# Kernel tuning notes

Measured on AMD Instinct MI355X. Metric: run time of the kernel, lower is better.

## Reference

```python
import jax, jax.numpy as jnp
import numpy as np

B, L, DIM = 8, 512, 8          # batch, seq len, raw channels (value dim D = 2*DIM = 16)
ET, HID, H = 128, 128, 2       # embed_time, hidden_size, num_heads
MAXLEN = 512
NEG = -1e9


def setup_inputs() -> dict:
    key = jax.random.key(0)
    ks = jax.random.split(key, 40)
    def n(i, shape, s=0.05):
        return jax.random.normal(ks[i], shape, jnp.float32) * s
    vals = jax.random.normal(ks[0], (B, L, DIM), jnp.float32)
    msk = (jax.random.uniform(ks[1], (B, L, DIM)) > 0.2).astype(jnp.float32)
    x = jnp.concatenate([vals, msk], -1)                      # (B, L, 2*DIM)
    time_steps = jax.random.uniform(ks[2], (B, L), jnp.float32)
    return {
        'x': x, 'time_steps': time_steps,
        # learned time embedding: Linear(1, ET-1) periodic + Linear(1,1)
        'w_per': n(3, (1, ET - 1)), 'b_per': n(4, (ET - 1,)),
        'w_lin': n(5, (1, 1)), 'b_lin': n(6, (1,)),
        # MultiTimeAttention projections
        'Wq_t': n(7, (ET, ET)), 'bq_t': n(8, (ET,)),
        'Wk_t': n(9, (ET, ET)), 'bk_t': n(10, (ET,)),
        'Wo_t': n(11, (2 * DIM * H, HID)), 'bo_t': n(12, (HID,)),
        'pos_emb': n(13, (MAXLEN + 1, HID)), 'cls_emb': n(14, (1, HID)),
        # transformer block (BERT-style post-LN encoder layer, d_ff=HID)
        'tWq': n(15, (HID, HID)), 'tbq': n(16, (HID,)),
        'tWk': n(17, (HID, HID)), 'tbk': n(18, (HID,)),
        'tWv': n(19, (HID, HID)), 'tbv': n(20, (HID,)),
        'tWo': n(21, (HID, HID)), 'tbo': n(22, (HID,)),
        'ln1_g': jnp.ones((HID,), jnp.float32), 'ln1_b': jnp.zeros((HID,), jnp.float32),
        'fW1': n(23, (HID, HID)), 'fb1': n(24, (HID,)),
        'fW2': n(25, (HID, HID)), 'fb2': n(26, (HID,)),
        'ln2_g': jnp.ones((HID,), jnp.float32), 'ln2_b': jnp.zeros((HID,), jnp.float32),
        # BertPooler
        'pW': n(27, (HID, HID)), 'pb': n(28, (HID,)),
    }


def _time_emb(tt, w_per, b_per, w_lin, b_lin):
    tt = tt[..., None]                                        # (B, L, 1)
    return jnp.concatenate([tt @ w_lin + b_lin, jnp.sin(tt @ w_per + b_per)], -1)


def _ln(x, g, b, eps=1e-5):
    m = x.mean(-1, keepdims=True)
    v = ((x - m) ** 2).mean(-1, keepdims=True)
    return (x - m) / jnp.sqrt(v + eps) * g + b


def _mta(q_emb, k_emb, value, mask, Wq, bq, Wk, bk, Wo, bo):
    # MultiTimeAttention: scores broadcast to value-channel axis, softmax over keys
    D = value.shape[-1]
    dk = ET // H
    def split(e, W, b):
        p = e @ W + b
        return p.reshape(e.shape[0], -1, H, dk).transpose(0, 2, 1, 3)
    q = split(q_emb, Wq, bq)                                  # (Bq, H, Lq, dk)
    k = split(k_emb, Wk, bk)                                  # (B,  H, Lk, dk)
    scores = jnp.matmul(q, k.swapaxes(-1, -2)) / jnp.sqrt(jnp.float32(dk))  # (B,H,Lq,Lk)
    s5 = jnp.where(mask[:, None, None, :, :] == 0, NEG, scores[..., None])  # (B,H,Lq,Lk,D)
    p = jax.nn.softmax(s5, axis=-2)
    out = jnp.einsum('bhqkd,bkd->bhqd', p, value)             # (B, H, Lq, D)
    Bv = value.shape[0]
    out = out.transpose(0, 2, 1, 3).reshape(Bv, -1, H * D)
    return out @ Wo + bo


def _tblock(x, tWq, tbq, tWk, tbk, tWv, tbv, tWo, tbo, ln1_g, ln1_b,
            fW1, fb1, fW2, fb2, ln2_g, ln2_b):
    Bq, Lq, _ = x.shape
    dk = HID // H
    def heads(W, b):
        return (x @ W + b).reshape(Bq, Lq, H, dk).transpose(0, 2, 1, 3)
    q, k, v = heads(tWq, tbq), heads(tWk, tbk), heads(tWv, tbv)
    a = jax.nn.softmax(jnp.matmul(q, k.swapaxes(-1, -2)) / jnp.sqrt(jnp.float32(dk)), -1)
    o = jnp.matmul(a, v).transpose(0, 2, 1, 3).reshape(Bq, Lq, HID) @ tWo + tbo
    x = _ln(x + o, ln1_g, ln1_b)
    f = jax.nn.relu(x @ fW1 + fb1) @ fW2 + fb2
    return _ln(x + f, ln2_g, ln2_b)


def reference(x, time_steps, w_per, b_per, w_lin, b_lin,
              Wq_t, bq_t, Wk_t, bk_t, Wo_t, bo_t, pos_emb, cls_emb,
              tWq, tbq, tWk, tbk, tWv, tbv, tWo, tbo, ln1_g, ln1_b,
              fW1, fb1, fW2, fb2, ln2_g, ln2_b, pW, pb):
    Bx = x.shape[0]
    mask_half = x[:, :, DIM:]
    mask = jnp.concatenate([mask_half, mask_half], -1)        # (B, L, 2*DIM)
    key_e = _time_emb(time_steps, w_per, b_per, w_lin, b_lin)
    tq_e = _time_emb(time_steps, w_per, b_per, w_lin, b_lin)  # query_time_steps=None -> same
    cls_t = jnp.linspace(0.0, 1.0, 128, dtype=jnp.float32)[None]
    cls_q_e = _time_emb(cls_t, w_per, b_per, w_lin, b_lin)    # (1, 128, ET)
    cls_out = _mta(cls_q_e, key_e, x, mask, Wq_t, bq_t, Wk_t, bk_t, Wo_t, bo_t)
    out = _mta(tq_e, key_e, x, mask, Wq_t, bq_t, Wk_t, bk_t, Wo_t, bo_t)
    tb = (tWq, tbq, tWk, tbk, tWv, tbv, tWo, tbo, ln1_g, ln1_b,
          fW1, fb1, fW2, fb2, ln2_g, ln2_b)
    cls_repr = jnp.broadcast_to(cls_emb[None, :, :], (Bx, 1, HID))
    # encode(cls_out, is_pooling=True), pooling='bert': no pos emb, take token 0
    h = _tblock(jnp.concatenate([cls_repr, cls_out], 1), *tb)
    cls_pooling = jnp.tanh(h[:, 0] @ pW + pb)                 # (B, HID)
    # encode(out, is_pooling=False) [pretrain path]: pos emb + transformer, drop CLS
    h2 = jnp.concatenate([cls_repr, out], 1)                  # (B, L+1, HID)
    h2 = h2 + pos_emb[:h2.shape[1]][None]
    h2 = _tblock(h2, *tb)
    last_hidden_state = h2[:, 1:]                             # (B, L, HID)
    return cls_pooling, last_hidden_state
```

## Files before the change

### kernel.cpp

```cpp
#include <hip/hip_runtime.h>
#include <hip/hip_bf16.h>
#include <math.h>


static constexpr int NM_ = 8 * 513;
static constexpr int NC_ = 8 * 129;
static constexpr int NT_ = NM_ + NC_;

using bf = __hip_bfloat16;
typedef __attribute__((ext_vector_type(8))) short bf16x8;
typedef __attribute__((ext_vector_type(4))) short bf16x4;
typedef __attribute__((ext_vector_type(4))) float floatx4;
typedef __attribute__((ext_vector_type(8))) unsigned short ushortx8;

__device__ __forceinline__ float wave_reduce_sum(float v) {
    #pragma unroll
    for (int off = 32; off >= 1; off >>= 1) v += __shfl_xor(v, off);
    return v;
}
__device__ __forceinline__ float wave_reduce_max(float v) {
    #pragma unroll
    for (int off = 32; off >= 1; off >>= 1) v = fmaxf(v, __shfl_xor(v, off));
    return v;
}
__device__ __forceinline__ float u2f(unsigned short u) {
    return __uint_as_float(((unsigned)u) << 16);
}
__device__ __forceinline__ unsigned short f2u(float f) {
    unsigned u = __float_as_uint(f);
    return (unsigned short)((u + 0x7FFF + ((u >> 16) & 1)) >> 16);
}
__device__ __forceinline__ bf16x8 join8(bf16x4 lo, bf16x4 hi) {
    return __builtin_shufflevector(lo, hi, 0, 1, 2, 3, 4, 5, 6, 7);
}
__device__ __forceinline__ float rdin(const void* p, int i, int flag) {
    return flag ? u2f(((const unsigned short*)p)[i]) : ((const float*)p)[i];
}

struct PrepAll {
    const void* src[32]; int n[32]; int dstoff[32];
    int cstart[32]; int cnum[32];
    int ncv;
    const void* wsrc[8]; unsigned short* wdst[8]; float wscale[8];
    const void* ts; const void* w_per; const void* b_per;
    const void* w_lin; const void* b_lin;
    unsigned short* key_e16;
    unsigned short* btg;
    const void* xsrc;
    const unsigned short* det;
};
__global__ void prep_all_kernel(PrepAll a, float* dst) {
    int flag = (a.det[0] == 0x3F80u) ? 1 : 0;
    int blk = blockIdx.x, tid = threadIdx.x;
    if (blk < a.ncv) {
        int which = -1, bi = 0;
        #pragma unroll
        for (int i = 0; i < 32; ++i)
            if (blk >= a.cstart[i] && blk < a.cstart[i] + a.cnum[i]) { which = i; bi = blk - a.cstart[i]; }
        if (which < 0) return;
        int i = bi * 256 + tid;
        if (i < a.n[which]) dst[a.dstoff[which] + i] = rdin(a.src[which], i, flag);
    } else if (blk < a.ncv + 512) {
        int p = blk - a.ncv;
        int m = p >> 6;
        int idx = (p & 63) * 256 + tid;
        int c = idx >> 9;
        int l = (idx >> 3) & 63;
        int j = idx & 7;
        int k = (c >> 3) * 32 + (l >> 4) * 8 + j;
        int n = (c & 7) * 16 + (l & 15);
        a.wdst[m][idx] = f2u(rdin(a.wsrc[m], k * 128 + n, flag) * a.wscale[m]);
    } else if (blk < a.ncv + 512 + 2112) {
        int p = blk - a.ncv - 512;
        int row = p * 2 + (tid >> 7), j = tid & 127;
        float t = (row < 4096) ? rdin(a.ts, row, flag)
                               : (float)(row - 4096) * (1.0f / 127.0f);
        float v;
        if (j == 0) v = t * rdin(a.w_lin, 0, flag) + rdin(a.b_lin, 0, flag);
        else        v = sinf(t * rdin(a.w_per, j - 1, flag) + rdin(a.b_per, j - 1, flag));
        a.key_e16[row * 128 + j] = f2u(v);
    } else {
        int p = blk - a.ncv - 512 - 2112;
        int e0 = (p * 256 + tid) * 8;
        int b = e0 >> 13;
        int c = (e0 >> 9) & 15;
        int k0 = e0 & 511;
        unsigned short out[8];
        #pragma unroll
        for (int j = 0; j < 8; ++j) {
            int k = k0 + j;
            float m = rdin(a.xsrc, (b * 512 + k) * 16 + 8 + (c & 7), flag);
            float val = (c < 8) ? rdin(a.xsrc, (b * 512 + k) * 16 + c, flag) * m : m;
            out[j] = f2u(val);
        }
        *(ushortx8*)(a.btg + e0) = *(ushortx8*)out;
    }
}

struct GemmM {
    const void* A[3]; const unsigned short* W[3]; const float* bias[3];
    unsigned short* C[3];
    int M[3]; float bscale[3];
};
__global__ void __launch_bounds__(256)
gemm_mfma_kernel(GemmM p) {
    int y = blockIdx.y;
    const unsigned short* Wsw = p.W[y];
    const float* bias = p.bias[y];
    unsigned short* C = p.C[y];
    int M = p.M[y];
    float bscale = p.bscale[y];
    int m0 = blockIdx.x * 16;
    if (m0 >= M) return;
    __shared__ unsigned short As[16][136];
    int tid = threadIdx.x;
    {
        const unsigned short* A = (const unsigned short*)p.A[y];
        int r = tid >> 4, c0 = (tid & 15) * 8;
        ushortx8 v = {0, 0, 0, 0, 0, 0, 0, 0};
        if (m0 + r < M) v = *(const ushortx8*)(A + (size_t)(m0 + r) * 128 + c0);
        *(ushortx8*)&As[r][c0] = v;
    }
    __syncthreads();

    int wv = tid >> 6, lane = tid & 63;
    floatx4 acc0 = {0.f, 0.f, 0.f, 0.f}, acc1 = acc0;
    int am = lane & 15, aq = lane >> 4;
    #pragma unroll
    for (int ks = 0; ks < 4; ++ks) {
        bf16x8 af = *(bf16x8*)&As[am][ks * 32 + aq * 8];
        const unsigned short* base = Wsw + ((size_t)ks * 8 + 2 * wv) * 512 + lane * 8;
        bf16x8 b0 = *(const bf16x8*)(base);
        bf16x8 b1 = *(const bf16x8*)(base + 512);
        acc0 = __builtin_amdgcn_mfma_f32_16x16x32_bf16(af, b0, acc0, 0, 0, 0);
        acc1 = __builtin_amdgcn_mfma_f32_16x16x32_bf16(af, b1, acc1, 0, 0, 0);
    }
    int col = lane & 15, rowb = (lane >> 4) * 4;
    #pragma unroll
    for (int t = 0; t < 2; ++t) {
        floatx4 acc = t ? acc1 : acc0;
        int n = wv * 32 + t * 16 + col;
        float bv = bias[n] * bscale;
        #pragma unroll
        for (int rg = 0; rg < 4; ++rg) {
            int m = m0 + rowb + rg;
            if (m < M) C[(size_t)m * 128 + n] = f2u(acc[rg] + bv);
        }
    }
}

__global__ void __launch_bounds__(256)
mta_att_part_kernel(const unsigned short* qp_cls, const unsigned short* qp_main,
                    const unsigned short* kp, const unsigned short* btg,
                    float* mpa, float* mma) {
    int F = blockIdx.x;
    int b = F & 7;
    int j2 = F >> 3;
    int ch = j2 & 1;
    int j = j2 >> 1;
    int h = j & 1;
    int xx = j >> 1;
    int is_cls = (xx >= 32);
    int qt = is_cls ? (xx - 32) : xx;
    int tid = threadIdx.x, lane = tid & 63, wv = tid >> 6;
    __shared__ unsigned short Qs[16][72];
    __shared__ unsigned short KV[64][72];
    __shared__ unsigned short sp[16][264];
    __shared__ float mrow[16];
    int q0 = qt * 16;
    int kg0 = ch * 256;

    if (tid < 128) {
        int r = tid >> 3, c0 = (tid & 7) * 8;
        const unsigned short* qrow = is_cls ? (qp_cls + (size_t)(q0 + r) * 128 + h * 64)
                                            : (qp_main + (size_t)(b * 512 + q0 + r) * 128 + h * 64);
        *(ushortx8*)&Qs[r][c0] = *(const ushortx8*)(qrow + c0);
    }
    __syncthreads();

    bf16x8 qf0, qf1;
    {
        int m = lane & 15, g = lane >> 4;
        qf0 = *(const bf16x8*)&Qs[m][g * 8];
        qf1 = *(const bf16x8*)&Qs[m][32 + g * 8];
    }

    for (int kt = 0; kt < 4; ++kt) {
        int k0 = kt * 64;
        {
            int kk = tid >> 3, e0 = (tid & 7) * 8;
            #pragma unroll
            for (int it = 0; it < 2; ++it, kk += 32)
                *(ushortx8*)&KV[kk][e0] =
                    *(const ushortx8*)(kp + (size_t)(b * 512 + kg0 + k0 + kk) * 128 + h * 64 + e0);
        }
        __syncthreads();
        int kn = lane & 15, g = lane >> 4;
        floatx4 acc = {0.f, 0.f, 0.f, 0.f};
        {
            bf16x8 b0 = *(const bf16x8*)&KV[wv * 16 + kn][g * 8];
            acc = __builtin_amdgcn_mfma_f32_16x16x32_bf16(qf0, b0, acc, 0, 0, 0);
            bf16x8 b1 = *(const bf16x8*)&KV[wv * 16 + kn][32 + g * 8];
            acc = __builtin_amdgcn_mfma_f32_16x16x32_bf16(qf1, b1, acc, 0, 0, 0);
        }
        int colk = k0 + wv * 16 + kn;
        #pragma unroll
        for (int rg = 0; rg < 4; ++rg) sp[g * 4 + rg][colk] = f2u(acc[rg]);
        __syncthreads();
    }

    for (int rr = wv; rr < 16; rr += 4) {
        float m = -1e30f;
        for (int k = lane; k < 256; k += 64) m = fmaxf(m, u2f(sp[rr][k]));
        m = wave_reduce_max(m);
        for (int k = lane; k < 256; k += 64) sp[rr][k] = f2u(expf(u2f(sp[rr][k]) - m));
        if (lane == 0) mrow[rr] = m;
    }
    __syncthreads();

    floatx4 macc = {0.f, 0.f, 0.f, 0.f};
    {
        int mq = lane & 15, g = lane >> 4;
        const unsigned short* bbase = btg + ((size_t)(b * 16 + mq)) * 512 + kg0 + g * 8;
        #pragma unroll
        for (int cc = 0; cc < 2; ++cc) {
            int koff = (wv + cc * 4) * 32;
            bf16x8 af = *(const bf16x8*)&sp[mq][koff + g * 8];
            bf16x8 bfv = *(const bf16x8*)(bbase + koff);
            macc = __builtin_amdgcn_mfma_f32_16x16x32_bf16(af, bfv, macc, 0, 0, 0);
        }
    }
    float* redC = (float*)&KV[0][0];
    float* Cfull = redC + 1024;
    #pragma unroll
    for (int rg = 0; rg < 4; ++rg) redC[(wv * 64 + lane) * 4 + rg] = macc[rg];
    __syncthreads();
    {
        int l = tid >> 2, rg = tid & 3;
        float s = redC[l * 4 + rg] + redC[(64 + l) * 4 + rg]
                + redC[(128 + l) * 4 + rg] + redC[(192 + l) * 4 + rg];
        int row = (l >> 4) * 4 + rg, c = l & 15;
        Cfull[row * 16 + c] = s;
    }
    __syncthreads();
    size_t pidx = ((size_t)(((b * 2 + h) * 40) + xx)) * 2 + ch;
    mpa[pidx * 256 + tid] = Cfull[tid];
    if (tid < 16) mma[pidx * 16 + tid] = mrow[tid];
}

__global__ void __launch_bounds__(256)
mta_qkv_kernel(const float* mpa, const float* mma,
               const float* Wo, const float* bo,
               const float* cls_emb, const float* pos, float* xin,
               const unsigned short* Wq, const unsigned short* Wk, const unsigned short* Wv,
               const float* bq, const float* bk, const float* bv_,
               unsigned short* outq, unsigned short* outk, unsigned short* outv) {
    int m0 = blockIdx.x * 16;
    __shared__ float As32[16][36];
    __shared__ unsigned short As[16][136];
    int tid = threadIdx.x;
    int r = tid >> 4, g = tid & 15, c0 = g * 8;

    int R = m0 + r;
    int srow, prow;
    if (R < NM_) {
        int b = R / 513, rr = R - b * 513;
        srow = (rr == 0) ? -1 : 1;
        prow = rr;
    } else {
        int mc = R - NM_;
        int b = mc / 129, rr = mc - b * 129;
        srow = (rr == 0) ? -1 : 1;
        prow = -1;
    }
    if (srow >= 0) {
        int hh = g >> 3, c = g & 7;
        int bb, xx2, lr2;
        if (R < NM_) {
            bb = R / 513; int ridx = R - bb * 513 - 1;
            xx2 = ridx >> 4; lr2 = ridx & 15;
        } else {
            int mc = R - NM_;
            bb = mc / 129; int ridx = mc - bb * 129 - 1;
            xx2 = 32 + (ridx >> 4); lr2 = ridx & 15;
        }
        size_t p0 = ((size_t)(((bb * 2 + hh) * 40) + xx2)) * 2;
        const float* C0 = mpa + (p0 + 0) * 256 + lr2 * 16;
        const float* C1 = mpa + (p0 + 1) * 256 + lr2 * 16;
        float m0v = mma[(p0 + 0) * 16 + lr2];
        float m1v = mma[(p0 + 1) * 16 + lr2];
        float mm = fmaxf(m0v, m1v);
        float e0 = expf(m0v - mm), e1 = expf(m1v - mm);
        float num = C0[c] * e0 + C1[c] * e1;
        float den = C0[8 + c] * e0 + C1[8 + c] * e1;
        As32[r][hh * 16 + c] = num / den;
        As32[r][hh * 16 + 8 + c] = 1.0f;
    }
    __syncthreads();

    float acc[8];
    if (srow < 0) {
        #pragma unroll
        for (int j = 0; j < 8; ++j) acc[j] = cls_emb[c0 + j];
    } else {
        #pragma unroll
        for (int j = 0; j < 8; ++j) acc[j] = bo[c0 + j];
        #pragma unroll 8
        for (int k = 0; k < 32; ++k) {
            float a = As32[r][k];
            const float4 w0 = *(const float4*)(Wo + (size_t)k * 128 + c0);
            const float4 w1 = *(const float4*)(Wo + (size_t)k * 128 + c0 + 4);
            acc[0] = fmaf(a, w0.x, acc[0]); acc[1] = fmaf(a, w0.y, acc[1]);
            acc[2] = fmaf(a, w0.z, acc[2]); acc[3] = fmaf(a, w0.w, acc[3]);
            acc[4] = fmaf(a, w1.x, acc[4]); acc[5] = fmaf(a, w1.y, acc[5]);
            acc[6] = fmaf(a, w1.z, acc[6]); acc[7] = fmaf(a, w1.w, acc[7]);
        }
    }
    if (prow >= 0) {
        const float* pr = pos + (size_t)prow * 128 + c0;
        float4 p0 = *(const float4*)(pr);
        float4 p1 = *(const float4*)(pr + 4);
        acc[0] += p0.x; acc[1] += p0.y; acc[2] += p0.z; acc[3] += p0.w;
        acc[4] += p1.x; acc[5] += p1.y; acc[6] += p1.z; acc[7] += p1.w;
    }
    *(float4*)(xin + (size_t)R * 128 + c0) = make_float4(acc[0], acc[1], acc[2], acc[3]);
    *(float4*)(xin + (size_t)R * 128 + c0 + 4) = make_float4(acc[4], acc[5], acc[6], acc[7]);
    *(ushort4*)&As[r][c0] = make_ushort4(f2u(acc[0]), f2u(acc[1]), f2u(acc[2]), f2u(acc[3]));
    *(ushort4*)&As[r][c0 + 4] = make_ushort4(f2u(acc[4]), f2u(acc[5]), f2u(acc[6]), f2u(acc[7]));
    __syncthreads();

    int wv = tid >> 6, lane = tid & 63;
    int am = lane & 15, aq = lane >> 4;
    int col = lane & 15, rowb = (lane >> 4) * 4;
    const unsigned short* Ws[3] = {Wq, Wk, Wv};
    const float* bs[3] = {bq, bk, bv_};
    float bsc[3] = {0.125f, 1.f, 1.f};
    unsigned short* Cs[3] = {outq, outk, outv};
    #pragma unroll
    for (int y = 0; y < 3; ++y) {
        floatx4 acc0 = {0.f, 0.f, 0.f, 0.f}, acc1 = acc0;
        #pragma unroll
        for (int ks = 0; ks < 4; ++ks) {
            bf16x8 af = *(bf16x8*)&As[am][ks * 32 + aq * 8];
            const unsigned short* base = Ws[y] + ((size_t)ks * 8 + 2 * wv) * 512 + lane * 8;
            bf16x8 b0 = *(const bf16x8*)(base);
            bf16x8 b1 = *(const bf16x8*)(base + 512);
            acc0 = __builtin_amdgcn_mfma_f32_16x16x32_bf16(af, b0, acc0, 0, 0, 0);
            acc1 = __builtin_amdgcn_mfma_f32_16x16x32_bf16(af, b1, acc1, 0, 0, 0);
        }
        #pragma unroll
        for (int t = 0; t < 2; ++t) {
            floatx4 a2 = t ? acc1 : acc0;
            int n = wv * 32 + t * 16 + col;
            float bvv = bs[y][n] * bsc[y];
            #pragma unroll
            for (int rg = 0; rg < 4; ++rg)
                Cs[y][(size_t)(m0 + rowb + rg) * 128 + n] = f2u(a2[rg] + bvv);
        }
    }
}

__global__ void __launch_bounds__(256)
tb_att_part_kernel(const unsigned short* qp, const unsigned short* kp,
                   const unsigned short* vp,
                   float* opm, float* mlm, float* opc, float* mlc) {
    int F = blockIdx.x;
    int b = F & 7;
    int j2 = F >> 3;
    int h = j2 & 1;
    int t = j2 >> 1;
    int is_cls = (t >= 99);
    int qt, ch;
    if (is_cls) { qt = t - 99; ch = 0; }
    else        { qt = t / 3;  ch = t - qt * 3; }
    int Lq = is_cls ? 129 : 513;
    int base = is_cls ? (4104 + b * 129) : (b * 513);
    int tid = threadIdx.x, lane = tid & 63, wv = tid >> 6;
    __shared__ unsigned short Qs[16][72];
    __shared__ unsigned short KV[64][72];
    __shared__ unsigned short sp[16][200];
    __shared__ float mrow[16], lrow[16];
    int q0 = qt * 16;
    int kg0 = ch * 192;

    if (tid < 128) {
        int r = tid >> 3, c0 = (tid & 7) * 8;
        int qr = q0 + r;
        ushortx8 v = {0, 0, 0, 0, 0, 0, 0, 0};
        if (qr < Lq) v = *(const ushortx8*)(qp + (size_t)(base + qr) * 128 + h * 64 + c0);
        *(ushortx8*)&Qs[r][c0] = v;
    }
    __syncthreads();

    bf16x8 qf0, qf1;
    {
        int m = lane & 15, g = lane >> 4;
        qf0 = *(const bf16x8*)&Qs[m][g * 8];
        qf1 = *(const bf16x8*)&Qs[m][32 + g * 8];
    }

    #pragma unroll
    for (int kt = 0; kt < 3; ++kt) {
        int k0 = kt * 64;
        {
            int kk = tid >> 3, e0 = (tid & 7) * 8;
            #pragma unroll
            for (int it = 0; it < 2; ++it, kk += 32) {
                int krow = kg0 + k0 + kk;
                ushortx8 v = {0, 0, 0, 0, 0, 0, 0, 0};
                if (krow < Lq) v = *(const ushortx8*)(kp + (size_t)(base + krow) * 128 + h * 64 + e0);
                *(ushortx8*)&KV[kk][e0] = v;
            }
        }
        __syncthreads();
        int kn = lane & 15, g = lane >> 4;
        floatx4 acc = {0.f, 0.f, 0.f, 0.f};
        {
            bf16x8 b0 = *(const bf16x8*)&KV[wv * 16 + kn][g * 8];
            acc = __builtin_amdgcn_mfma_f32_16x16x32_bf16(qf0, b0, acc, 0, 0, 0);
            bf16x8 b1 = *(const bf16x8*)&KV[wv * 16 + kn][32 + g * 8];
            acc = __builtin_amdgcn_mfma_f32_16x16x32_bf16(qf1, b1, acc, 0, 0, 0);
        }
        int colk = k0 + wv * 16 + kn;
        #pragma unroll
        for (int rg = 0; rg < 4; ++rg)
            sp[g * 4 + rg][colk] = f2u((kg0 + colk < Lq) ? acc[rg] : -1e30f);
        __syncthreads();
    }

    for (int rr = wv; rr < 16; rr += 4) {
        float m = -1e30f;
        #pragma unroll
        for (int k = 0; k < 3; ++k) m = fmaxf(m, u2f(sp[rr][k * 64 + lane]));
        m = wave_reduce_max(m);
        float sum = 0.f;
        #pragma unroll
        for (int k = 0; k < 3; ++k) {
            float e = expf(u2f(sp[rr][k * 64 + lane]) - m);
            sp[rr][k * 64 + lane] = f2u(e);
            sum += e;
        }
        sum = wave_reduce_sum(sum);
        if (lane == 0) { mrow[rr] = m; lrow[rr] = sum; }
    }

    floatx4 oacc = {0.f, 0.f, 0.f, 0.f};
    #pragma unroll
    for (int kt = 0; kt < 3; ++kt) {
        int k0 = kt * 64;
        __syncthreads();
        {
            int kk = tid & 31, e0 = (tid >> 5) * 8;
            #pragma unroll
            for (int it = 0; it < 2; ++it, kk += 32) {
                int krow = kg0 + k0 + kk;
                ushortx8 v = {0, 0, 0, 0, 0, 0, 0, 0};
                if (krow < Lq) v = *(const ushortx8*)(vp + (size_t)(base + krow) * 128 + h * 64 + e0);
                #pragma unroll
                for (int j3 = 0; j3 < 8; ++j3) KV[e0 + j3][kk] = v[j3];
            }
        }
        __syncthreads();
        int dn = lane & 15, g = lane >> 4;
        #pragma unroll
        for (int c = 0; c < 2; ++c) {
            bf16x4 plo = *(const bf16x4*)&sp[lane & 15][k0 + c * 32 + g * 8];
            bf16x4 phi = *(const bf16x4*)&sp[lane & 15][k0 + c * 32 + g * 8 + 4];
            bf16x8 vf = *(const bf16x8*)&KV[wv * 16 + dn][c * 32 + g * 8];
            oacc = __builtin_amdgcn_mfma_f32_16x16x32_bf16(join8(plo, phi), vf, oacc, 0, 0, 0);
        }
    }
    float* op = is_cls ? (opc + ((size_t)((b * 2 + h) * 9 + qt)) * 1024)
                       : (opm + ((size_t)(((b * 2 + h) * 33 + qt) * 3 + ch)) * 1024);
    int dcol = wv * 16 + (lane & 15), g = lane >> 4;
    #pragma unroll
    for (int rg = 0; rg < 4; ++rg) {
        int q = g * 4 + rg;
        op[q * 64 + dcol] = oacc[rg];
    }
    if (tid < 16) {
        float* ml = is_cls ? (mlc + ((size_t)((b * 2 + h) * 9 + qt)) * 32)
                           : (mlm + ((size_t)(((b * 2 + h) * 33 + qt) * 3 + ch)) * 32);
        ml[tid * 2]     = mrow[tid];
        ml[tid * 2 + 1] = lrow[tid];
    }
}

__global__ void __launch_bounds__(256)
attnout_ffn_kernel(const float* opm, const float* mlm,
                   const float* opc, const float* mlc,
                   const unsigned short* Wao, const float* bao,
                   const float* resid, const float* g1, const float* b1ln,
                   const unsigned short* W1, const float* fb1,
                   const unsigned short* W2, const float* fb2,
                   const float* g2, const float* b2ln,
                   const float* pW, const float* pb, float* dout) {
    int m0 = blockIdx.x * 16;
    __shared__ unsigned short As[16][136];
    __shared__ float Xs[16][128];
    __shared__ unsigned short Hs[16][136];
    __shared__ float redS[4][4][4], redQ[4][4][4];
    __shared__ float smean[16], sinv[16];
    __shared__ float x2row[128];
    __shared__ int poolb;
    int tid = threadIdx.x;
    if (tid == 0) poolb = -1;
    {
        int r = tid >> 4, c0 = (tid & 15) * 8;
        int R = m0 + r;
        int iscl, bb, rr;
        if (R < NM_) { bb = R / 513; rr = R - bb * 513; iscl = 0; }
        else { int mc = R - NM_; bb = mc / 129; rr = mc - bb * 129; iscl = 1; }
        int qt = rr >> 4, lr = rr & 15;
        int hh = c0 >> 6, d0 = c0 & 63;
        float vals[8];
        if (iscl) {
            size_t pb2 = (size_t)((bb * 2 + hh) * 9 + qt);
            const float* op = opc + pb2 * 1024 + lr * 64 + d0;
            float linv = 1.f / mlc[pb2 * 32 + lr * 2 + 1];
            #pragma unroll
            for (int jj = 0; jj < 8; ++jj) vals[jj] = op[jj] * linv;
        } else {
            size_t pb2 = (size_t)(((bb * 2 + hh) * 33 + qt) * 3);
            const float* op0 = opm + (pb2 + 0) * 1024 + lr * 64 + d0;
            const float* op1 = opm + (pb2 + 1) * 1024 + lr * 64 + d0;
            const float* op2 = opm + (pb2 + 2) * 1024 + lr * 64 + d0;
            float m0v = mlm[(pb2 + 0) * 32 + lr * 2];
            float m1v = mlm[(pb2 + 1) * 32 + lr * 2];
            float m2v = mlm[(pb2 + 2) * 32 + lr * 2];
            float l0 = mlm[(pb2 + 0) * 32 + lr * 2 + 1];
            float l1 = mlm[(pb2 + 1) * 32 + lr * 2 + 1];
            float l2 = mlm[(pb2 + 2) * 32 + lr * 2 + 1];
            float mm = fmaxf(fmaxf(m0v, m1v), m2v);
            float e0 = expf(m0v - mm), e1 = expf(m1v - mm), e2 = expf(m2v - mm);
            float linv = 1.f / (l0 * e0 + l1 * e1 + l2 * e2);
            #pragma unroll
            for (int jj = 0; jj < 8; ++jj)
                vals[jj] = (op0[jj] * e0 + op1[jj] * e1 + op2[jj] * e2) * linv;
        }
        unsigned short o8[8];
        #pragma unroll
        for (int jj = 0; jj < 8; ++jj) o8[jj] = f2u(vals[jj]);
        *(ushortx8*)&As[r][c0] = *(ushortx8*)o8;
    }
    __syncthreads();

    int wv = tid >> 6, lane = tid & 63;
    int am = lane & 15, aq = lane >> 4;
    int col = lane & 15, g = lane >> 4, rowb = g * 4;

    float ov[2][4];
    {
        floatx4 acc0 = {0.f, 0.f, 0.f, 0.f}, acc1 = acc0;
        #pragma unroll
        for (int ks = 0; ks < 4; ++ks) {
            bf16x8 af = *(bf16x8*)&As[am][ks * 32 + aq * 8];
            const unsigned short* base = Wao + ((size_t)ks * 8 + 2 * wv) * 512 + lane * 8;
            bf16x8 bb0 = *(const bf16x8*)(base);
            bf16x8 bb1 = *(const bf16x8*)(base + 512);
            acc0 = __builtin_amdgcn_mfma_f32_16x16x32_bf16(af, bb0, acc0, 0, 0, 0);
            acc1 = __builtin_amdgcn_mfma_f32_16x16x32_bf16(af, bb1, acc1, 0, 0, 0);
        }
        #pragma unroll
        for (int t = 0; t < 2; ++t) {
            int n = wv * 32 + t * 16 + col;
            float bv = bao[n];
            floatx4 acc = t ? acc1 : acc0;
            #pragma unroll
            for (int rg = 0; rg < 4; ++rg)
                ov[t][rg] = acc[rg] + bv + resid[(size_t)(m0 + rowb + rg) * 128 + n];
        }
    }
    #pragma unroll
    for (int rg = 0; rg < 4; ++rg) {
        float s = ov[0][rg] + ov[1][rg];
        float q = ov[0][rg] * ov[0][rg] + ov[1][rg] * ov[1][rg];
        #pragma unroll
        for (int off = 8; off >= 1; off >>= 1) {
            s += __shfl_xor(s, off);
            q += __shfl_xor(q, off);
        }
        if ((lane & 15) == 0) { redS[wv][g][rg] = s; redQ[wv][g][rg] = q; }
    }
    __syncthreads();
    if (tid < 16) {
        int gg = tid >> 2, rg = tid & 3;
        float s = redS[0][gg][rg] + redS[1][gg][rg] + redS[2][gg][rg] + redS[3][gg][rg];
        float q = redQ[0][gg][rg] + redQ[1][gg][rg] + redQ[2][gg][rg] + redQ[3][gg][rg];
        float mean = s * 0.0078125f;
        float var = q * 0.0078125f - mean * mean;
        smean[tid] = mean;
        sinv[tid] = rsqrtf(var + 1e-5f);
    }
    __syncthreads();
    #pragma unroll
    for (int t = 0; t < 2; ++t) {
        int n = wv * 32 + t * 16 + col;
        float gm = g1[n], bb = b1ln[n];
        #pragma unroll
        for (int rg = 0; rg < 4; ++rg) {
            int row = rowb + rg;
            float val = (ov[t][rg] - smean[row]) * sinv[row] * gm + bb;
            Xs[row][n] = val;
            As[row][n] = f2u(val);
        }
    }
    __syncthreads();

    {
        floatx4 acc0 = {0.f, 0.f, 0.f, 0.f}, acc1 = acc0;
        #pragma unroll
        for (int ks = 0; ks < 4; ++ks) {
            bf16x8 af = *(bf16x8*)&As[am][ks * 32 + aq * 8];
            const unsigned short* base = W1 + ((size_t)ks * 8 + 2 * wv) * 512 + lane * 8;
            bf16x8 bb0 = *(const bf16x8*)(base);
            bf16x8 bb1 = *(const bf16x8*)(base + 512);
            acc0 = __builtin_amdgcn_mfma_f32_16x16x32_bf16(af, bb0, acc0, 0, 0, 0);
            acc1 = __builtin_amdgcn_mfma_f32_16x16x32_bf16(af, bb1, acc1, 0, 0, 0);
        }
        #pragma unroll
        for (int t = 0; t < 2; ++t) {
            int n = wv * 32 + t * 16 + col;
            float bv = fb1[n];
            floatx4 acc = t ? acc1 : acc0;
            #pragma unroll
            for (int rg = 0; rg < 4; ++rg)
                Hs[rowb + rg][n] = f2u(fmaxf(acc[rg] + bv, 0.f));
        }
    }
    __syncthreads();

    floatx4 acc0 = {0.f, 0.f, 0.f, 0.f}, acc1 = acc0;
    #pragma unroll
    for (int ks = 0; ks < 4; ++ks) {
        bf16x8 af = *(bf16x8*)&Hs[am][ks * 32 + aq * 8];
        const unsigned short* base = W2 + ((size_t)ks * 8 + 2 * wv) * 512 + lane * 8;
        bf16x8 bb0 = *(const bf16x8*)(base);
        bf16x8 bb1 = *(const bf16x8*)(base + 512);
        acc0 = __builtin_amdgcn_mfma_f32_16x16x32_bf16(af, bb0, acc0, 0, 0, 0);
        acc1 = __builtin_amdgcn_mfma_f32_16x16x32_bf16(af, bb1, acc1, 0, 0, 0);
    }
    #pragma unroll
    for (int t = 0; t < 2; ++t) {
        int n = wv * 32 + t * 16 + col;
        float bv = fb2[n];
        floatx4 acc = t ? acc1 : acc0;
        #pragma unroll
        for (int rg = 0; rg < 4; ++rg)
            ov[t][rg] = acc[rg] + bv + Xs[rowb + rg][n];
    }
    #pragma unroll
    for (int rg = 0; rg < 4; ++rg) {
        float s = ov[0][rg] + ov[1][rg];
        float q = ov[0][rg] * ov[0][rg] + ov[1][rg] * ov[1][rg];
        #pragma unroll
        for (int off = 8; off >= 1; off >>= 1) {
            s += __shfl_xor(s, off);
            q += __shfl_xor(q, off);
        }
        if ((lane & 15) == 0) { redS[wv][g][rg] = s; redQ[wv][g][rg] = q; }
    }
    __syncthreads();
    if (tid < 16) {
        int gg = tid >> 2, rg = tid & 3;
        float s = redS[0][gg][rg] + redS[1][gg][rg] + redS[2][gg][rg] + redS[3][gg][rg];
        float q = redQ[0][gg][rg] + redQ[1][gg][rg] + redQ[2][gg][rg] + redQ[3][gg][rg];
        float mean = s * 0.0078125f;
        float var = q * 0.0078125f - mean * mean;
        smean[tid] = mean;
        sinv[tid] = rsqrtf(var + 1e-5f);
    }
    __syncthreads();
    #pragma unroll
    for (int t = 0; t < 2; ++t) {
        int n = wv * 32 + t * 16 + col;
        float gm = g2[n], bb = b2ln[n];
        #pragma unroll
        for (int rg = 0; rg < 4; ++rg) {
            int row = rowb + rg;
            int m = m0 + row;
            float val = (ov[t][rg] - smean[row]) * sinv[row] * gm + bb;
            if (m < NM_) {
                int b = m / 513, r2 = m - b * 513;
                if (r2 >= 1)
                    dout[1024 + (size_t)b * 65536 + (size_t)(r2 - 1) * 128 + n] = val;
            } else {
                int mc = m - NM_;
                int b = mc / 129, r2 = mc - b * 129;
                if (r2 == 0) {
                    x2row[n] = val;
                    if (n == 0) poolb = b;
                }
            }
        }
    }
    __syncthreads();
    if (poolb >= 0 && tid < 128) {
        float acc = pb[tid];
        for (int k = 0; k < 128; ++k) acc = fmaf(x2row[k], pW[(size_t)k * 128 + tid], acc);
        dout[(size_t)poolb * 128 + tid] = tanhf(acc);
    }
}

extern "C" void kernel_launch(void* const* d_in, const int* in_sizes, int n_in,
                              void* d_out, int out_size, void* d_ws, size_t ws_size,
                              hipStream_t stream) {
    float* w = (float*)d_ws;
    size_t off = 0;
    auto alloc = [&](size_t n) {
        float* p = w + off;
        off += (n + 3) & ~(size_t)3;
        return p;
    };
    auto allocU = [&](size_t n) { return (unsigned short*)alloc((n + 1) / 2); };

    PrepAll pa{};
    int nn = n_in < 32 ? n_in : 32;
    float* fin[32];
    const int needconv[32] = {0,0,0,0,0,0, 0,1, 0,1, 1,1, 1,1, 0,1, 0,1, 0,1,
                              0,1, 1,1, 0,1, 0,1, 1,1, 1,1};
    int ncv = 0;
    for (int i = 0; i < nn; ++i) {
        pa.src[i] = d_in[i];
        pa.n[i] = in_sizes[i];
        fin[i] = alloc(in_sizes[i]);
        pa.dstoff[i] = (int)(fin[i] - w);
        if (needconv[i]) {
            int nb = (in_sizes[i] + 255) / 256;
            pa.cstart[i] = ncv;
            pa.cnum[i] = nb;
            ncv += nb;
        } else { pa.cstart[i] = -1; pa.cnum[i] = 0; }
    }
    for (int i = nn; i < 32; ++i) {
        pa.src[i] = nullptr; pa.n[i] = 0; pa.dstoff[i] = 0;
        pa.cstart[i] = -1; pa.cnum[i] = 0;
    }
    pa.ncv = ncv;

    const float* bq_t    = fin[7];
    const float* bk_t    = fin[9];
    const float* Wo_t    = fin[10]; const float* bo_t = fin[11];
    const float* pos_emb = fin[12]; const float* cls_emb = fin[13];
    const float* tbq = fin[15]; const float* tbk = fin[17]; const float* tbv = fin[19];
    const float* tbo = fin[21];
    const float* ln1_g = fin[22]; const float* ln1_b = fin[23];
    const float* fb1 = fin[25]; const float* fb2 = fin[27];
    const float* ln2_g = fin[28]; const float* ln2_b = fin[29];
    const float* pW = fin[30]; const float* pb = fin[31];

    const int widx[8] = {8, 6, 14, 16, 18, 20, 24, 26};
    unsigned short* wsw[8];
    for (int i = 0; i < 8; ++i) {
        wsw[i] = allocU(16384);
        pa.wsrc[i] = d_in[widx[i]];
        pa.wdst[i] = wsw[i];
        pa.wscale[i] = (i == 1 || i == 2) ? 0.125f : 1.0f;
    }
    pa.ts = d_in[1]; pa.w_per = d_in[2]; pa.b_per = d_in[3];
    pa.w_lin = d_in[4]; pa.b_lin = d_in[5];
    pa.xsrc = d_in[0];
    pa.det = (const unsigned short*)d_in[22];

    unsigned short* key_e16 = allocU(4224 * 128);
    unsigned short* cls_e16 = key_e16 + 4096 * 128;
    pa.key_e16 = key_e16;
    unsigned short* btg = allocU(8 * 16 * 512);
    pa.btg = btg;

    unsigned short* qp_main16 = allocU(4096 * 128);
    unsigned short* kp_main16 = allocU(4096 * 128);
    unsigned short* qp_cls16  = allocU(128 * 128);
    float* mpa = alloc(1280 * 256);
    float* mma = alloc(1280 * 16);
    float* opm = alloc((size_t)1584 * 1024);
    float* mlm = alloc(1584 * 32);
    float* opc = alloc((size_t)144 * 1024);
    float* mlc = alloc(144 * 32);
    float* xin = alloc((size_t)NT_ * 128);
    unsigned short* tbq16 = allocU((size_t)NT_ * 128);
    unsigned short* tbk16 = allocU((size_t)NT_ * 128);
    unsigned short* tbv16 = allocU((size_t)NT_ * 128);
    (void)ws_size;

    float* outf = (float*)d_out;

    prep_all_kernel<<<ncv + 512 + 2112 + 32, 256, 0, stream>>>(pa, w);

    {
        GemmM p{};
        p.A[0] = key_e16; p.W[0] = wsw[0]; p.bias[0] = bk_t; p.C[0] = kp_main16;
        p.M[0] = 4096; p.bscale[0] = 1.f;
        p.A[1] = key_e16; p.W[1] = wsw[1]; p.bias[1] = bq_t; p.C[1] = qp_main16;
        p.M[1] = 4096; p.bscale[1] = 0.125f;
        p.A[2] = cls_e16; p.W[2] = wsw[1]; p.bias[2] = bq_t; p.C[2] = qp_cls16;
        p.M[2] = 128; p.bscale[2] = 0.125f;
        gemm_mfma_kernel<<<dim3(256, 3), 256, 0, stream>>>(p);
    }

    mta_att_part_kernel<<<1280, 256, 0, stream>>>(qp_cls16, qp_main16, kp_main16,
                                                  btg, mpa, mma);

    mta_qkv_kernel<<<321, 256, 0, stream>>>(mpa, mma, Wo_t, bo_t, cls_emb, pos_emb, xin,
                                            wsw[2], wsw[3], wsw[4], tbq, tbk, tbv,
                                            tbq16, tbk16, tbv16);

    tb_att_part_kernel<<<1728, 256, 0, stream>>>(tbq16, tbk16, tbv16,
                                                 opm, mlm, opc, mlc);

    attnout_ffn_kernel<<<321, 256, 0, stream>>>(opm, mlm, opc, mlc,
                                                wsw[5], tbo, xin, ln1_g, ln1_b,
                                                wsw[6], fb1, wsw[7], fb2, ln2_g, ln2_b,
                                                pW, pb, outf);
}
```

Measured before the change: 179.5 us.

## Split attention key dimension into finer chunks for more parallel blocks

The MTA attention kernel now splits keys into 4 chunks of 128 instead of 2 of 256, and the transformer attention kernel uses 64-key chunks (9 for the main sequence, 3 for CLS) instead of 192-key chunks, so each block loads K and V only once. The combine stages in mta_qkv and attnout_ffn become generic loops over the chunks with a log-sum-exp merge. This raises the block count (2560 and 5184) and shortens each block's serial loop. The cost is larger partial buffers, more combine work and extra global traffic. Fast __sinf and __expf intrinsics replace sinf and expf, which slightly lowers accuracy.

Result: slower. 185.4 us (+3.3%).

```diff
diff --git a/kernel.cpp b/kernel.cpp
--- a/kernel.cpp
+++ b/kernel.cpp
@@ -77,7 +77,7 @@
                                : (float)(row - 4096) * (1.0f / 127.0f);
         float v;
         if (j == 0) v = t * rdin(a.w_lin, 0, flag) + rdin(a.b_lin, 0, flag);
-        else        v = sinf(t * rdin(a.w_per, j - 1, flag) + rdin(a.b_per, j - 1, flag));
+        else        v = __sinf(t * rdin(a.w_per, j - 1, flag) + rdin(a.b_per, j - 1, flag));
         a.key_e16[row * 128 + j] = f2u(v);
     } else {
         int p = blk - a.ncv - 512 - 2112;
@@ -156,8 +156,8 @@
     int F = blockIdx.x;
     int b = F & 7;
     int j2 = F >> 3;
-    int ch = j2 & 1;
-    int j = j2 >> 1;
+    int ch = j2 & 3;
+    int j = j2 >> 2;
     int h = j & 1;
     int xx = j >> 1;
     int is_cls = (xx >= 32);
@@ -165,10 +165,10 @@
     int tid = threadIdx.x, lane = tid & 63, wv = tid >> 6;
     __shared__ unsigned short Qs[16][72];
     __shared__ unsigned short KV[64][72];
-    __shared__ unsigned short sp[16][264];
+    __shared__ unsigned short sp[16][136];
     __shared__ float mrow[16];
     int q0 = qt * 16;
-    int kg0 = ch * 256;
+    int kg0 = ch * 128;
 
     if (tid < 128) {
         int r = tid >> 3, c0 = (tid & 7) * 8;
@@ -185,7 +185,8 @@
         qf1 = *(const bf16x8*)&Qs[m][32 + g * 8];
     }
 
-    for (int kt = 0; kt < 4; ++kt) {
+    #pragma unroll
+    for (int kt = 0; kt < 2; ++kt) {
         int k0 = kt * 64;
         {
             int kk = tid >> 3, e0 = (tid & 7) * 8;
@@ -211,9 +212,12 @@
 
     for (int rr = wv; rr < 16; rr += 4) {
         float m = -1e30f;
-        for (int k = lane; k < 256; k += 64) m = fmaxf(m, u2f(sp[rr][k]));
+        #pragma unroll
+        for (int k = 0; k < 2; ++k) m = fmaxf(m, u2f(sp[rr][k * 64 + lane]));
         m = wave_reduce_max(m);
-        for (int k = lane; k < 256; k += 64) sp[rr][k] = f2u(expf(u2f(sp[rr][k]) - m));
+        #pragma unroll
+        for (int k = 0; k < 2; ++k)
+            sp[rr][k * 64 + lane] = f2u(__expf(u2f(sp[rr][k * 64 + lane]) - m));
         if (lane == 0) mrow[rr] = m;
     }
     __syncthreads();
@@ -222,13 +226,10 @@
     {
         int mq = lane & 15, g = lane >> 4;
         const unsigned short* bbase = btg + ((size_t)(b * 16 + mq)) * 512 + kg0 + g * 8;
-        #pragma unroll
-        for (int cc = 0; cc < 2; ++cc) {
-            int koff = (wv + cc * 4) * 32;
-            bf16x8 af = *(const bf16x8*)&sp[mq][koff + g * 8];
-            bf16x8 bfv = *(const bf16x8*)(bbase + koff);
-            macc = __builtin_amdgcn_mfma_f32_16x16x32_bf16(af, bfv, macc, 0, 0, 0);
-        }
+        int koff = wv * 32;
+        bf16x8 af = *(const bf16x8*)&sp[mq][koff + g * 8];
+        bf16x8 bfv = *(const bf16x8*)(bbase + koff);
+        macc = __builtin_amdgcn_mfma_f32_16x16x32_bf16(af, bfv, macc, 0, 0, 0);
     }
     float* redC = (float*)&KV[0][0];
     float* Cfull = redC + 1024;
@@ -243,7 +244,7 @@
         Cfull[row * 16 + c] = s;
     }
     __syncthreads();
-    size_t pidx = ((size_t)(((b * 2 + h) * 40) + xx)) * 2 + ch;
+    size_t pidx = ((size_t)(((b * 2 + h) * 40) + xx)) * 4 + ch;
     mpa[pidx * 256 + tid] = Cfull[tid];
     if (tid < 16) mma[pidx * 16 + tid] = mrow[tid];
 }
@@ -284,15 +285,22 @@
             bb = mc / 129; int ridx = mc - bb * 129 - 1;
             xx2 = 32 + (ridx >> 4); lr2 = ridx & 15;
         }
-        size_t p0 = ((size_t)(((bb * 2 + hh) * 40) + xx2)) * 2;
-        const float* C0 = mpa + (p0 + 0) * 256 + lr2 * 16;
-        const float* C1 = mpa + (p0 + 1) * 256 + lr2 * 16;
-        float m0v = mma[(p0 + 0) * 16 + lr2];
-        float m1v = mma[(p0 + 1) * 16 + lr2];
-        float mm = fmaxf(m0v, m1v);
-        float e0 = expf(m0v - mm), e1 = expf(m1v - mm);
-        float num = C0[c] * e0 + C1[c] * e1;
-        float den = C0[8 + c] * e0 + C1[8 + c] * e1;
+        size_t p0 = ((size_t)(((bb * 2 + hh) * 40) + xx2)) * 4;
+        float mv[4];
+        float mm = -1e30f;
+        #pragma unroll
+        for (int i = 0; i < 4; ++i) {
+            mv[i] = mma[(p0 + i) * 16 + lr2];
+            mm = fmaxf(mm, mv[i]);
+        }
+        float num = 0.f, den = 0.f;
+        #pragma unroll
+        for (int i = 0; i < 4; ++i) {
+            float e = __expf(mv[i] - mm);
+            const float* Ci = mpa + (p0 + i) * 256 + lr2 * 16;
+            num += Ci[c] * e;
+            den += Ci[8 + c] * e;
+        }
         As32[r][hh * 16 + c] = num / den;
         As32[r][hh * 16 + 8 + c] = 1.0f;
     }
@@ -369,19 +377,19 @@
     int j2 = F >> 3;
     int h = j2 & 1;
     int t = j2 >> 1;
-    int is_cls = (t >= 99);
+    int is_cls = (t >= 297);
     int qt, ch;
-    if (is_cls) { qt = t - 99; ch = 0; }
-    else        { qt = t / 3;  ch = t - qt * 3; }
+    if (is_cls) { int tc = t - 297; qt = tc / 3; ch = tc - qt * 3; }
+    else        { qt = t / 9; ch = t - qt * 9; }
     int Lq = is_cls ? 129 : 513;
     int base = is_cls ? (4104 + b * 129) : (b * 513);
     int tid = threadIdx.x, lane = tid & 63, wv = tid >> 6;
     __shared__ unsigned short Qs[16][72];
     __shared__ unsigned short KV[64][72];
-    __shared__ unsigned short sp[16][200];
+    __shared__ unsigned short sp[16][72];
     __shared__ float mrow[16], lrow[16];
     int q0 = qt * 16;
-    int kg0 = ch * 192;
+    int kg0 = ch * 64;
 
     if (tid < 128) {
         int r = tid >> 3, c0 = (tid & 7) * 8;
@@ -390,6 +398,16 @@
         if (qr < Lq) v = *(const ushortx8*)(qp + (size_t)(base + qr) * 128 + h * 64 + c0);
         *(ushortx8*)&Qs[r][c0] = v;
     }
+    {
+        int kk = tid >> 3, e0 = (tid & 7) * 8;
+        #pragma unroll
+        for (int it = 0; it < 2; ++it, kk += 32) {
+            int krow = kg0 + kk;
+            ushortx8 v = {0, 0, 0, 0, 0, 0, 0, 0};
+            if (krow < Lq) v = *(const ushortx8*)(kp + (size_t)(base + krow) * 128 + h * 64 + e0);
+            *(ushortx8*)&KV[kk][e0] = v;
+        }
+    }
     __syncthreads();
 
     bf16x8 qf0, qf1;
@@ -398,80 +416,55 @@
         qf0 = *(const bf16x8*)&Qs[m][g * 8];
         qf1 = *(const bf16x8*)&Qs[m][32 + g * 8];
     }
-
-    #pragma unroll
-    for (int kt = 0; kt < 3; ++kt) {
-        int k0 = kt * 64;
-        {
-            int kk = tid >> 3, e0 = (tid & 7) * 8;
-            #pragma unroll
-            for (int it = 0; it < 2; ++it, kk += 32) {
-                int krow = kg0 + k0 + kk;
-                ushortx8 v = {0, 0, 0, 0, 0, 0, 0, 0};
-                if (krow < Lq) v = *(const ushortx8*)(kp + (size_t)(base + krow) * 128 + h * 64 + e0);
-                *(ushortx8*)&KV[kk][e0] = v;
-            }
-        }
-        __syncthreads();
+    {
         int kn = lane & 15, g = lane >> 4;
         floatx4 acc = {0.f, 0.f, 0.f, 0.f};
-        {
-            bf16x8 b0 = *(const bf16x8*)&KV[wv * 16 + kn][g * 8];
-            acc = __builtin_amdgcn_mfma_f32_16x16x32_bf16(qf0, b0, acc, 0, 0, 0);
-            bf16x8 b1 = *(const bf16x8*)&KV[wv * 16 + kn][32 + g * 8];
-            acc = __builtin_amdgcn_mfma_f32_16x16x32_bf16(qf1, b1, acc, 0, 0, 0);
-        }
-        int colk = k0 + wv * 16 + kn;
+        bf16x8 b0 = *(const bf16x8*)&KV[wv * 16 + kn][g * 8];
+        acc = __builtin_amdgcn_mfma_f32_16x16x32_bf16(qf0, b0, acc, 0, 0, 0);
+        bf16x8 b1 = *(const bf16x8*)&KV[wv * 16 + kn][32 + g * 8];
+        acc = __builtin_amdgcn_mfma_f32_16x16x32_bf16(qf1, b1, acc, 0, 0, 0);
+        int colk = wv * 16 + kn;
         #pragma unroll
         for (int rg = 0; rg < 4; ++rg)
             sp[g * 4 + rg][colk] = f2u((kg0 + colk < Lq) ? acc[rg] : -1e30f);
-        __syncthreads();
-    }
+    }
+    __syncthreads();
 
     for (int rr = wv; rr < 16; rr += 4) {
-        float m = -1e30f;
-        #pragma unroll
-        for (int k = 0; k < 3; ++k) m = fmaxf(m, u2f(sp[rr][k * 64 + lane]));
-        m = wave_reduce_max(m);
-        float sum = 0.f;
-        #pragma unroll
-        for (int k = 0; k < 3; ++k) {
-            float e = expf(u2f(sp[rr][k * 64 + lane]) - m);
-            sp[rr][k * 64 + lane] = f2u(e);
-            sum += e;
-        }
-        sum = wave_reduce_sum(sum);
+        float m = wave_reduce_max(u2f(sp[rr][lane]));
+        float e = __expf(u2f(sp[rr][lane]) - m);
+        sp[rr][lane] = f2u(e);
+        float sum = wave_reduce_sum(e);
         if (lane == 0) { mrow[rr] = m; lrow[rr] = sum; }
     }
+    __syncthreads();
+
+    {
+        int kk = tid & 31, e0 = (tid >> 5) * 8;
+        #pragma unroll
+        for (int it = 0; it < 2; ++it, kk += 32) {
+            int krow = kg0 + kk;
+            ushortx8 v = {0, 0, 0, 0, 0, 0, 0, 0};
+            if (krow < Lq) v = *(const ushortx8*)(vp + (size_t)(base + krow) * 128 + h * 64 + e0);
+            #pragma unroll
+            for (int j3 = 0; j3 < 8; ++j3) KV[e0 + j3][kk] = v[j3];
+        }
+    }
+    __syncthreads();
 
     floatx4 oacc = {0.f, 0.f, 0.f, 0.f};
-    #pragma unroll
-    for (int kt = 0; kt < 3; ++kt) {
-        int k0 = kt * 64;
-        __syncthreads();
-        {
-            int kk = tid & 31, e0 = (tid >> 5) * 8;
-            #pragma unroll
-            for (int it = 0; it < 2; ++it, kk += 32) {
-                int krow = kg0 + k0 + kk;
-                ushortx8 v = {0, 0, 0, 0, 0, 0, 0, 0};
-                if (krow < Lq) v = *(const ushortx8*)(vp + (size_t)(base + krow) * 128 + h * 64 + e0);
-                #pragma unroll
-                for (int j3 = 0; j3 < 8; ++j3) KV[e0 + j3][kk] = v[j3];
-            }
-        }
-        __syncthreads();
+    {
         int dn = lane & 15, g = lane >> 4;
         #pragma unroll
         for (int c = 0; c < 2; ++c) {
-            bf16x4 plo = *(const bf16x4*)&sp[lane & 15][k0 + c * 32 + g * 8];
-            bf16x4 phi = *(const bf16x4*)&sp[lane & 15][k0 + c * 32 + g * 8 + 4];
+            bf16x4 plo = *(const bf16x4*)&sp[lane & 15][c * 32 + g * 8];
+            bf16x4 phi = *(const bf16x4*)&sp[lane & 15][c * 32 + g * 8 + 4];
             bf16x8 vf = *(const bf16x8*)&KV[wv * 16 + dn][c * 32 + g * 8];
             oacc = __builtin_amdgcn_mfma_f32_16x16x32_bf16(join8(plo, phi), vf, oacc, 0, 0, 0);
         }
     }
-    float* op = is_cls ? (opc + ((size_t)((b * 2 + h) * 9 + qt)) * 1024)
-                       : (opm + ((size_t)(((b * 2 + h) * 33 + qt) * 3 + ch)) * 1024);
+    float* op = is_cls ? (opc + ((size_t)(((b * 2 + h) * 9 + qt) * 3 + ch)) * 1024)
+                       : (opm + ((size_t)(((b * 2 + h) * 33 + qt) * 9 + ch)) * 1024);
     int dcol = wv * 16 + (lane & 15), g = lane >> 4;
     #pragma unroll
     for (int rg = 0; rg < 4; ++rg) {
@@ -479,8 +472,8 @@
         op[q * 64 + dcol] = oacc[rg];
     }
     if (tid < 16) {
-        float* ml = is_cls ? (mlc + ((size_t)((b * 2 + h) * 9 + qt)) * 32)
-                           : (mlm + ((size_t)(((b * 2 + h) * 33 + qt) * 3 + ch)) * 32);
+        float* ml = is_cls ? (mlc + ((size_t)(((b * 2 + h) * 9 + qt) * 3 + ch)) * 32)
+                           : (mlm + ((size_t)(((b * 2 + h) * 33 + qt) * 9 + ch)) * 32);
         ml[tid * 2]     = mrow[tid];
         ml[tid * 2 + 1] = lrow[tid];
     }
@@ -513,34 +506,27 @@
         else { int mc = R - NM_; bb = mc / 129; rr = mc - bb * 129; iscl = 1; }
         int qt = rr >> 4, lr = rr & 15;
         int hh = c0 >> 6, d0 = c0 & 63;
-        float vals[8];
-        if (iscl) {
-            size_t pb2 = (size_t)((bb * 2 + hh) * 9 + qt);
-            const float* op = opc + pb2 * 1024 + lr * 64 + d0;
-            float linv = 1.f / mlc[pb2 * 32 + lr * 2 + 1];
+        int nch = iscl ? 3 : 9;
+        size_t pb2;
+        const float* opb; const float* mlb;
+        if (iscl) { pb2 = (size_t)((bb * 2 + hh) * 9 + qt) * 3; opb = opc; mlb = mlc; }
+        else      { pb2 = (size_t)((bb * 2 + hh) * 33 + qt) * 9; opb = opm; mlb = mlm; }
+        float mm = -1e30f;
+        for (int i = 0; i < nch; ++i)
+            mm = fmaxf(mm, mlb[(pb2 + i) * 32 + lr * 2]);
+        float vals[8] = {0.f, 0.f, 0.f, 0.f, 0.f, 0.f, 0.f, 0.f};
+        float den = 0.f;
+        for (int i = 0; i < nch; ++i) {
+            float e = __expf(mlb[(pb2 + i) * 32 + lr * 2] - mm);
+            den += mlb[(pb2 + i) * 32 + lr * 2 + 1] * e;
+            const float* op = opb + (pb2 + i) * 1024 + lr * 64 + d0;
             #pragma unroll
-            for (int jj = 0; jj < 8; ++jj) vals[jj] = op[jj] * linv;
-        } else {
-            size_t pb2 = (size_t)(((bb * 2 + hh) * 33 + qt) * 3);
-            const float* op0 = opm + (pb2 + 0) * 1024 + lr * 64 + d0;
-            const float* op1 = opm + (pb2 + 1) * 1024 + lr * 64 + d0;
-            const float* op2 = opm + (pb2 + 2) * 1024 + lr * 64 + d0;
-            float m0v = mlm[(pb2 + 0) * 32 + lr * 2];
-            float m1v = mlm[(pb2 + 1) * 32 + lr * 2];
-            float m2v = mlm[(pb2 + 2) * 32 + lr * 2];
-            float l0 = mlm[(pb2 + 0) * 32 + lr * 2 + 1];
-            float l1 = mlm[(pb2 + 1) * 32 + lr * 2 + 1];
-            float l2 = mlm[(pb2 + 2) * 32 + lr * 2 + 1];
-            float mm = fmaxf(fmaxf(m0v, m1v), m2v);
-            float e0 = expf(m0v - mm), e1 = expf(m1v - mm), e2 = expf(m2v - mm);
-            float linv = 1.f / (l0 * e0 + l1 * e1 + l2 * e2);
-            #pragma unroll
-            for (int jj = 0; jj < 8; ++jj)
-                vals[jj] = (op0[jj] * e0 + op1[jj] * e1 + op2[jj] * e2) * linv;
-        }
+            for (int jj = 0; jj < 8; ++jj) vals[jj] += op[jj] * e;
+        }
+        float linv = 1.f / den;
         unsigned short o8[8];
         #pragma unroll
-        for (int jj = 0; jj < 8; ++jj) o8[jj] = f2u(vals[jj]);
+        for (int jj = 0; jj < 8; ++jj) o8[jj] = f2u(vals[jj] * linv);
         *(ushortx8*)&As[r][c0] = *(ushortx8*)o8;
     }
     __syncthreads();
@@ -771,12 +757,12 @@
     unsigned short* qp_main16 = allocU(4096 * 128);
     unsigned short* kp_main16 = allocU(4096 * 128);
     unsigned short* qp_cls16  = allocU(128 * 128);
-    float* mpa = alloc(1280 * 256);
-    float* mma = alloc(1280 * 16);
-    float* opm = alloc((size_t)1584 * 1024);
-    float* mlm = alloc(1584 * 32);
-    float* opc = alloc((size_t)144 * 1024);
-    float* mlc = alloc(144 * 32);
+    float* mpa = alloc((size_t)2560 * 256);
+    float* mma = alloc(2560 * 16);
+    float* opm = alloc((size_t)4752 * 1024);
+    float* mlm = alloc(4752 * 32);
+    float* opc = alloc((size_t)432 * 1024);
+    float* mlc = alloc(432 * 32);
     float* xin = alloc((size_t)NT_ * 128);
     unsigned short* tbq16 = allocU((size_t)NT_ * 128);
     unsigned short* tbk16 = allocU((size_t)NT_ * 128);
@@ -798,14 +784,14 @@
         gemm_mfma_kernel<<<dim3(256, 3), 256, 0, stream>>>(p);
     }
 
-    mta_att_part_kernel<<<1280, 256, 0, stream>>>(qp_cls16, qp_main16, kp_main16,
+    mta_att_part_kernel<<<2560, 256, 0, stream>>>(qp_cls16, qp_main16, kp_main16,
                                                   btg, mpa, mma);
 
     mta_qkv_kernel<<<321, 256, 0, stream>>>(mpa, mma, Wo_t, bo_t, cls_emb, pos_emb, xin,
                                             wsw[2], wsw[3], wsw[4], tbq, tbk, tbv,
                                             tbq16, tbk16, tbv16);
 
-    tb_att_part_kernel<<<1728, 256, 0, stream>>>(tbq16, tbk16, tbv16,
+    tb_att_part_kernel<<<5184, 256, 0, stream>>>(tbq16, tbk16, tbv16,
                                                  opm, mlm, opc, mlc);
 
     attnout_ffn_kernel<<<321, 256, 0, stream>>>(opm, mlm, opc, mlc,
```
